# Kernel optimization log

Measured on AMD Instinct MI355X. Metric: run time of the kernel, lower is better.

Reference implementation:

```python
import jax, jax.numpy as jnp
import numpy as np

N_HEAD = 16
HEAD_DIM = 128  # n_embd // n_head
RMS_EPS = 1.1920929e-07  # torch.finfo(float32).eps, F.rms_norm default
ROPE_BASE = 10000.0


def _rope_tables(T, head_dim, dtype=jnp.float32):
    half = head_dim // 2
    inv_freq = 1.0 / (ROPE_BASE ** (jnp.arange(half, dtype=jnp.float32) / half))
    t = jnp.arange(T, dtype=jnp.float32)
    freqs = jnp.outer(t, inv_freq)  # [T, half]
    return jnp.cos(freqs).astype(dtype), jnp.sin(freqs).astype(dtype)


def _apply_rope(x, cos, sin):
    # x: [B, T, H, D]; cos/sin: [T, D//2]
    half = x.shape[-1] // 2
    x1, x2 = x[..., :half], x[..., half:]
    c = cos[None, :, None, :]
    s = sin[None, :, None, :]
    return jnp.concatenate([x1 * c - x2 * s, x1 * s + x2 * c], axis=-1)


def _rms_norm(x):
    ms = jnp.mean(jnp.square(x), axis=-1, keepdims=True)
    return x * jax.lax.rsqrt(ms + RMS_EPS)


def setup_inputs() -> dict:
    key = jax.random.key(0)
    ks = jax.random.split(key, 5)
    B, T, E = 4, 2048, 2048
    x = jax.random.normal(ks[0], (B, T, E), dtype=jnp.float32)
    scale = 0.02
    wq = jax.random.normal(ks[1], (E, E), dtype=jnp.float32) * scale
    wk = jax.random.normal(ks[2], (E, E), dtype=jnp.float32) * scale
    wv = jax.random.normal(ks[3], (E, E), dtype=jnp.float32) * scale
    wo = jax.random.normal(ks[4], (E, E), dtype=jnp.float32) * scale
    return {"x": x, "wq": wq, "wk": wk, "wv": wv, "wo": wo}


def reference(x, wq, wk, wv, wo):
    B, T, E = x.shape
    H, D = N_HEAD, HEAD_DIM
    # QKV projections (bias-free linears)
    q = (x @ wq).reshape(B, T, H, D)
    k = (x @ wk).reshape(B, T, H, D)
    v = (x @ wv).reshape(B, T, H, D)
    # RoPE then parameter-free QK RMS norm
    cos, sin = _rope_tables(T, D, x.dtype)
    q = _rms_norm(_apply_rope(q, cos, sin))
    k = _rms_norm(_apply_rope(k, cos, sin))
    # causal SDPA
    scale = 1.0 / jnp.sqrt(jnp.asarray(D, dtype=x.dtype))
    scores = jnp.einsum('bqhd,bkhd->bhqk', q, k) * scale
    causal = jnp.tril(jnp.ones((T, T), dtype=bool))
    scores = jnp.where(causal[None, None], scores, jnp.asarray(-jnp.inf, scores.dtype))
    attn = jax.nn.softmax(scores, axis=-1)
    y = jnp.einsum('bhqk,bkhd->bqhd', attn, v).reshape(B, T, E)
    return y @ wo
```

## Files before the change

kernel.cpp:

```cpp
#include <hip/hip_runtime.h>
#include <math.h>

#define T_SEQ 2048
#define BATCH 4
#define E_DIM 2048
#define NHEAD 16
#define HDIM 128
#define RMS_EPS 1.1920929e-07f
#define NQT (T_SEQ / 128)

typedef unsigned short u16;
typedef __attribute__((ext_vector_type(8))) unsigned short u16x8;
typedef __attribute__((ext_vector_type(8))) short bf16x8;
typedef __attribute__((ext_vector_type(4))) float f32x4;

typedef const __attribute__((address_space(1))) unsigned int g_u32;
typedef __attribute__((address_space(3))) unsigned int l_u32;

static __device__ __forceinline__ u16 f2b(float f) {
  unsigned int u = __builtin_bit_cast(unsigned int, f);
  u += 0x7fffu + ((u >> 16) & 1u);
  return (u16)(u >> 16);
}
static __device__ __forceinline__ float b2f(u16 v) {
  return __builtin_bit_cast(float, ((unsigned int)v) << 16);
}

__global__ __launch_bounds__(256) void convert_f32_bf16(
    const float* __restrict__ src, u16* __restrict__ dst, int n) {
  int i = (blockIdx.x * 256 + threadIdx.x) * 4;
  if (i >= n) return;
  float4 v = *reinterpret_cast<const float4*>(src + i);
  ushort4 o;
  o.x = f2b(v.x); o.y = f2b(v.y); o.z = f2b(v.z); o.w = f2b(v.w);
  *reinterpret_cast<ushort4*>(dst + i) = o;
}

__global__ __launch_bounds__(256) void convt_w_k(
    const float* __restrict__ W, u16* __restrict__ Wt) {
  __shared__ u16 tile[64][72];
  int c0 = blockIdx.x * 64;
  int r0 = blockIdx.y * 64;
  int tid = threadIdx.x;
  int lrow = tid >> 2;
  int lcol = (tid & 3) * 16;
#pragma unroll
  for (int i = 0; i < 4; ++i) {
    float4 v = *reinterpret_cast<const float4*>(
        W + (long long)(r0 + lrow) * E_DIM + c0 + lcol + i * 4);
    tile[lrow][lcol + i * 4 + 0] = f2b(v.x);
    tile[lrow][lcol + i * 4 + 1] = f2b(v.y);
    tile[lrow][lcol + i * 4 + 2] = f2b(v.z);
    tile[lrow][lcol + i * 4 + 3] = f2b(v.w);
  }
  __syncthreads();
  int wrow = tid >> 2;
  int wcol = (tid & 3) * 16;
  u16 o[16];
#pragma unroll
  for (int i = 0; i < 16; ++i) o[i] = tile[wcol + i][wrow];
  u16* dst = Wt + (long long)(c0 + wrow) * E_DIM + r0 + wcol;
  *reinterpret_cast<u16x8*>(dst)     = *reinterpret_cast<u16x8*>(&o[0]);
  *reinterpret_cast<u16x8*>(dst + 8) = *reinterpret_cast<u16x8*>(&o[8]);
}

__global__ __launch_bounds__(256) void rope_tables_k(
    float* __restrict__ cost, float* __restrict__ sint) {
  int idx = blockIdx.x * 256 + threadIdx.x;
  int i = idx & 63, t = idx >> 6;
  double inv = pow(10000.0, -(double)i / 64.0);
  double ang = (double)t * inv;
  cost[idx] = (float)cos(ang);
  sint[idx] = (float)sin(ang);
}

__global__ __launch_bounds__(256) void rope_rms_k(
    u16* __restrict__ Qb, u16* __restrict__ Kb, const float* __restrict__ cost,
    const float* __restrict__ sint) {
  int half = gridDim.x >> 1;
  int isK = blockIdx.x >= half;
  u16* qk = isK ? Kb : Qb;
  float outscale = isK ? 1.0f : 0.08838834764831845f;
  int wave = threadIdx.x >> 6;
  int lane = threadIdx.x & 63;
  long long row = (long long)(blockIdx.x - (isK ? half : 0)) * 4 + wave;
  int th = (int)(row >> 4);
  int t = th & (T_SEQ - 1);
  u16* p = qk + row * HDIM;
  float x1 = b2f(p[lane]);
  float x2 = b2f(p[lane + 64]);
  float c = cost[t * 64 + lane];
  float s = sint[t * 64 + lane];
  float o1 = x1 * c - x2 * s;
  float o2 = x1 * s + x2 * c;
  float ss = o1 * o1 + o2 * o2;
#pragma unroll
  for (int m = 32; m >= 1; m >>= 1) ss += __shfl_xor(ss, m, 64);
  float r = rsqrtf(ss * (1.0f / 128.0f) + RMS_EPS) * outscale;
  p[lane] = f2b(o1 * r);
  p[lane + 64] = f2b(o2 * r);
}

__global__ __launch_bounds__(256) void transpose_v_k(
    const u16* __restrict__ V, u16* __restrict__ Vt) {
  __shared__ u16 tile[64][72];
  int t0 = blockIdx.x * 64, d0 = blockIdx.y * 64;
  int bh = blockIdx.z;
  int b = bh >> 4, h = bh & 15;
  int tid = threadIdx.x;
  int lrow = tid >> 3;
  int lcol = (tid & 7) * 8;
#pragma unroll
  for (int pass = 0; pass < 2; ++pass) {
    int row = lrow + pass * 32;
    const u16* src = V + ((((long long)b * T_SEQ + t0 + row) * NHEAD + h) << 7) + d0 + lcol;
    *reinterpret_cast<u16x8*>(&tile[row][lcol]) = *reinterpret_cast<const u16x8*>(src);
  }
  __syncthreads();
#pragma unroll
  for (int pass = 0; pass < 2; ++pass) {
    int drow = (tid >> 3) + pass * 32;
    int tcol = (tid & 7) * 8;
    u16x8 o;
#pragma unroll
    for (int i = 0; i < 8; ++i) o[i] = tile[tcol + i][drow];
    u16* dst = Vt + ((long long)bh * HDIM + d0 + drow) * T_SEQ + t0 + tcol;
    *reinterpret_cast<u16x8*>(dst) = o;
  }
}

__global__ __launch_bounds__(512, 2) void gemm_bt_k(
    const u16* __restrict__ A,
    const u16* __restrict__ Bt0, const u16* __restrict__ Bt1, const u16* __restrict__ Bt2,
    u16* __restrict__ C0, u16* __restrict__ C1, u16* __restrict__ C2,
    float* __restrict__ Cf, int M, int N, int K) {
  int lin = blockIdx.x + (blockIdx.y << 3) + (blockIdx.z << 8);
  int kx = lin & 7, ii = lin >> 3;
  int by = ((kx >> 1) << 3) + (ii & 7);
  int bx, bz;
  if (gridDim.z == 3) {
    int u = (kx & 1) * 12 + (ii >> 3);
    bx = u & 7; bz = u >> 3;
  } else {
    bx = ((kx & 1) << 2) + (ii >> 3);
    bz = 0;
  }
  const u16* Bt = bz == 0 ? Bt0 : (bz == 1 ? Bt1 : Bt2);
  u16* C = bz == 0 ? C0 : (bz == 1 ? C1 : C2);

  __shared__ u16 As[2][256 * 64];
  __shared__ u16 Bs[2][256 * 64];
  const int tid = threadIdx.x;
  const int lane = tid & 63, wave = tid >> 6;
  const int wm = wave >> 2, wn = wave & 3;
  const int m0 = by * 256, n0 = bx * 256;
  const int lr = lane & 15, lq = lane >> 4, l7 = lane & 7;
  const int NT = K >> 6;

  int rowA[2][2], rowB[2][2];
  const u16* gA[2][2];
  const u16* gB[2][2];
#pragma unroll
  for (int l = 0; l < 2; ++l) {
    int rihb = l * 64 + wave * 8;
#pragma unroll
    for (int h = 0; h < 2; ++h) {
      int ra = ((rihb >> 6) << 7) + h * 64 + (rihb & 63);
      int rb = ((rihb >> 5) << 6) + h * 32 + (rihb & 31);
      rowA[h][l] = ra;
      rowB[h][l] = rb;
      int rA = ra + (lane >> 3);
      int rB = rb + (lane >> 3);
      gA[h][l] = A + (long long)(m0 + rA) * K + ((l7 ^ (rA & 7)) * 8);
      gB[h][l] = Bt + (long long)(n0 + rB) * K + ((l7 ^ (rB & 7)) * 8);
    }
  }

  f32x4 acc[8][4] = {};

#define GLDS(gp, lp) \
  __builtin_amdgcn_global_load_lds((g_u32*)(gp), (l_u32*)(lp), 16, 0, 0)
#define LD_A(mt, ks)                                                          \
  (*reinterpret_cast<const bf16x8*>(                                          \
      Ab + (wm * 128 + (mt) * 16 + lr) * 64 + ((((ks) << 2) + lq) ^ l7) * 8))
#define LD_B(nt, ks)                                                          \
  (*reinterpret_cast<const bf16x8*>(                                          \
      Bb + (wn * 64 + (nt) * 16 + lr) * 64 + ((((ks) << 2) + lq) ^ l7) * 8))
#define MFMA_PH(ph)                                                           \
  _Pragma("unroll") for (int mi = 0; mi < 2; ++mi)                            \
  _Pragma("unroll") for (int ni = 0; ni < 4; ++ni)                            \
  _Pragma("unroll") for (int ks = 0; ks < 2; ++ks)                            \
    acc[(ph) * 2 + mi][ni] = __builtin_amdgcn_mfma_f32_16x16x32_bf16(         \
        aA[mi][ks], bB[ni][ks], acc[(ph) * 2 + mi][ni], 0, 0, 0);

  GLDS(gB[0][0], &Bs[0][rowB[0][0] * 64]); GLDS(gB[0][1], &Bs[0][rowB[0][1] * 64]);
  GLDS(gB[1][0], &Bs[0][rowB[1][0] * 64]); GLDS(gB[1][1], &Bs[0][rowB[1][1] * 64]);
  GLDS(gA[0][0], &As[0][rowA[0][0] * 64]); GLDS(gA[0][1], &As[0][rowA[0][1] * 64]);
  GLDS(gA[1][0], &As[0][rowA[1][0] * 64]); GLDS(gA[1][1], &As[0][rowA[1][1] * 64]);
  GLDS(gB[0][0] + 64, &Bs[1][rowB[0][0] * 64]); GLDS(gB[0][1] + 64, &Bs[1][rowB[0][1] * 64]);
  GLDS(gB[1][0] + 64, &Bs[1][rowB[1][0] * 64]); GLDS(gB[1][1] + 64, &Bs[1][rowB[1][1] * 64]);
  GLDS(gA[0][0] + 64, &As[1][rowA[0][0] * 64]); GLDS(gA[0][1] + 64, &As[1][rowA[0][1] * 64]);
  asm volatile("s_waitcnt vmcnt(6)" ::: "memory");
  __builtin_amdgcn_s_barrier();
  __builtin_amdgcn_sched_barrier(0);

  for (int t = 0; t < NT; ++t) {
    const u16* Ab = As[t & 1];
    const u16* Bb = Bs[t & 1];
    u16* An = (u16*)As[(t & 1) ^ 1];
    u16* Ac = (u16*)As[t & 1];
    u16* Bc = (u16*)Bs[t & 1];
    const bool g1 = (t + 1 < NT), g2 = (t + 2 < NT);
    bf16x8 aA[2][2], bB[4][2];

#pragma unroll
    for (int mi = 0; mi < 2; ++mi) { aA[mi][0] = LD_A(mi, 0); aA[mi][1] = LD_A(mi, 1); }
#pragma unroll
    for (int ni = 0; ni < 4; ++ni) { bB[ni][0] = LD_B(ni, 0); bB[ni][1] = LD_B(ni, 1); }
    if (g1) {
      GLDS(gA[1][0] + 64, &An[rowA[1][0] * 64]);
      GLDS(gA[1][1] + 64, &An[rowA[1][1] * 64]);
    }
    asm volatile("s_waitcnt lgkmcnt(8)" ::: "memory");
    __builtin_amdgcn_s_barrier();
    asm volatile("s_waitcnt lgkmcnt(0)" ::: "memory");
    __builtin_amdgcn_sched_barrier(0);
    __builtin_amdgcn_s_setprio(1);
    MFMA_PH(0);
    __builtin_amdgcn_s_setprio(0);
    __builtin_amdgcn_s_barrier();

#pragma unroll
    for (int mi = 0; mi < 2; ++mi) { aA[mi][0] = LD_A(2 + mi, 0); aA[mi][1] = LD_A(2 + mi, 1); }
    if (g2) {
      GLDS(gB[0][0] + 128, &Bc[rowB[0][0] * 64]);
      GLDS(gB[0][1] + 128, &Bc[rowB[0][1] * 64]);
    }
    __builtin_amdgcn_s_barrier();
    asm volatile("s_waitcnt lgkmcnt(0)" ::: "memory");
    __builtin_amdgcn_sched_barrier(0);
    __builtin_amdgcn_s_setprio(1);
    MFMA_PH(1);
    __builtin_amdgcn_s_setprio(0);
    __builtin_amdgcn_s_barrier();

#pragma unroll
    for (int mi = 0; mi < 2; ++mi) { aA[mi][0] = LD_A(4 + mi, 0); aA[mi][1] = LD_A(4 + mi, 1); }
    if (g2) {
      GLDS(gB[1][0] + 128, &Bc[rowB[1][0] * 64]);
      GLDS(gB[1][1] + 128, &Bc[rowB[1][1] * 64]);
    }
    __builtin_amdgcn_s_barrier();
    asm volatile("s_waitcnt lgkmcnt(0)" ::: "memory");
    __builtin_amdgcn_sched_barrier(0);
    __builtin_amdgcn_s_setprio(1);
    MFMA_PH(2);
    __builtin_amdgcn_s_setprio(0);
    __builtin_amdgcn_s_barrier();

#pragma unroll
    for (int mi = 0; mi < 2; ++mi) { aA[mi][0] = LD_A(6 + mi, 0); aA[mi][1] = LD_A(6 + mi, 1); }
    if (g2) {
      GLDS(gA[0][0] + 128, &Ac[rowA[0][0] * 64]);
      GLDS(gA[0][1] + 128, &Ac[rowA[0][1] * 64]);
    }
    __builtin_amdgcn_s_barrier();
    asm volatile("s_waitcnt lgkmcnt(0)" ::: "memory");
    __builtin_amdgcn_sched_barrier(0);
    __builtin_amdgcn_s_setprio(1);
    MFMA_PH(3);
    __builtin_amdgcn_s_setprio(0);
    if (t < NT - 2) {
      asm volatile("s_waitcnt vmcnt(6)" ::: "memory");
    } else {
      asm volatile("s_waitcnt vmcnt(0)" ::: "memory");
    }
    __builtin_amdgcn_s_barrier();
    __builtin_amdgcn_sched_barrier(0);

#pragma unroll
    for (int l = 0; l < 2; ++l)
#pragma unroll
      for (int h = 0; h < 2; ++h) { gA[h][l] += 64; gB[h][l] += 64; }
  }
#undef LD_A
#undef LD_B
#undef MFMA_PH
#undef GLDS

#pragma unroll
  for (int mt = 0; mt < 8; ++mt)
#pragma unroll
    for (int nt = 0; nt < 4; ++nt) {
      long long col = n0 + wn * 64 + nt * 16 + lr;
#pragma unroll
      for (int r = 0; r < 4; ++r) {
        long long row = m0 + wm * 128 + mt * 16 + lq * 4 + r;
        float v = acc[mt][nt][r];
        if (Cf) Cf[row * N + col] = v;
        else C[row * N + col] = f2b(v);
      }
    }
}

__global__ __launch_bounds__(256, 3) void attn_k(
    const u16* __restrict__ Q, const u16* __restrict__ K,
    const u16* __restrict__ Vt, u16* __restrict__ Y) {
  __shared__ u16 Ks[64 * 128];
  __shared__ u16 Vs[128 * 64];
  __shared__ u16 Ps[4][32 * 72];
  __shared__ float Al[4][32];
  int lin = blockIdx.x + (blockIdx.y << 3);
  int pair = (lin >> 6);
  int bh = ((lin & 7) << 3) + ((lin >> 3) & 7);
  int b = bh >> 4, h = bh & 15;
  int tid = threadIdx.x, lane = tid & 63, wave = tid >> 6;
  int lr = lane & 15, lq = lane >> 4;

  const u16* kp[4];
  const u16* vp[4];
#pragma unroll
  for (int p = 0; p < 4; ++p) {
    int c = p * 256 + wave * 64 + lane;
    int key = c >> 4, sk = c & 15, gk = (sk - key) & 15;
    kp[p] = K + (((long long)b * T_SEQ + key) * NHEAD + h) * HDIM + gk * 8;
    int d = c >> 3, sv = c & 7, gv = (sv - d) & 7;
    vp[p] = Vt + ((long long)bh * HDIM + d) * T_SEQ + gv * 8;
  }

#pragma unroll 1
  for (int phase = 0; phase < 2; ++phase) {
    int qt = phase == 0 ? (NQT - 1 - pair) : pair;
    int qbase = qt * 128 + wave * 32;

    bf16x8 aq[2][4];
#pragma unroll
    for (int n2 = 0; n2 < 2; ++n2) {
      const u16* qp = Q + (((long long)b * T_SEQ + qbase + n2 * 16 + lr) * NHEAD + h) * HDIM;
#pragma unroll
      for (int kt = 0; kt < 4; ++kt)
        aq[n2][kt] = *reinterpret_cast<const bf16x8*>(qp + kt * 32 + lq * 8);
    }

    float m_s[2], l_s[2];
#pragma unroll
    for (int n2 = 0; n2 < 2; ++n2) { m_s[n2] = -INFINITY; l_s[n2] = 0.f; }
    f32x4 o[2][8] = {};

    int niter = 2 * qt + 2;
    for (int j = 0; j < niter; ++j) {
      __syncthreads();
#pragma unroll
      for (int p = 0; p < 4; ++p) {
        __builtin_amdgcn_global_load_lds(
            (g_u32*)(kp[p] + (long long)j * 64 * NHEAD * HDIM),
            (l_u32*)(Ks + p * 2048 + wave * 512), 16, 0, 0);
        __builtin_amdgcn_global_load_lds(
            (g_u32*)(vp[p] + j * 64),
            (l_u32*)(Vs + p * 2048 + wave * 512), 16, 0, 0);
      }
      __syncthreads();

      f32x4 s[4][2];
#pragma unroll
      for (int mt = 0; mt < 4; ++mt) {
        int key = mt * 16 + lr;
        bf16x8 ak[4];
#pragma unroll
        for (int kt = 0; kt < 4; ++kt) {
          int slot = (kt * 4 + lq + key) & 15;
          ak[kt] = *reinterpret_cast<const bf16x8*>(&Ks[key * 128 + slot * 8]);
        }
#pragma unroll
        for (int n2 = 0; n2 < 2; ++n2) {
          f32x4 acc = {};
#pragma unroll
          for (int kt = 0; kt < 4; ++kt)
            acc = __builtin_amdgcn_mfma_f32_16x16x32_bf16(ak[kt], aq[n2][kt], acc, 0, 0, 0);
          s[mt][n2] = acc;
        }
      }

      if (j >= 2 * qt) {
#pragma unroll
        for (int mt = 0; mt < 4; ++mt)
#pragma unroll
          for (int n2 = 0; n2 < 2; ++n2) {
            int q = qbase + n2 * 16 + lr;
#pragma unroll
            for (int r = 0; r < 4; ++r) {
              int key = j * 64 + mt * 16 + lq * 4 + r;
              if (key > q) s[mt][n2][r] = -INFINITY;
            }
          }
      }

      float alpha[2];
#pragma unroll
      for (int n2 = 0; n2 < 2; ++n2) {
        float mx = s[0][n2][0];
#pragma unroll
        for (int mt = 0; mt < 4; ++mt)
#pragma unroll
          for (int r = 0; r < 4; ++r) mx = fmaxf(mx, s[mt][n2][r]);
        mx = fmaxf(mx, __shfl_xor(mx, 16, 64));
        mx = fmaxf(mx, __shfl_xor(mx, 32, 64));
        float mn = fmaxf(m_s[n2], mx);
        alpha[n2] = __expf(m_s[n2] - mn);
        m_s[n2] = mn;
        float sum = 0.f;
        int q = n2 * 16 + lr;
#pragma unroll
        for (int mt = 0; mt < 4; ++mt) {
          ushort4 pk;
          float p0 = __expf(s[mt][n2][0] - mn);
          float p1 = __expf(s[mt][n2][1] - mn);
          float p2 = __expf(s[mt][n2][2] - mn);
          float p3 = __expf(s[mt][n2][3] - mn);
          sum += (p0 + p1) + (p2 + p3);
          pk.x = f2b(p0); pk.y = f2b(p1); pk.z = f2b(p2); pk.w = f2b(p3);
          *reinterpret_cast<ushort4*>(&Ps[wave][q * 72 + mt * 16 + lq * 4]) = pk;
        }
        sum += __shfl_xor(sum, 16, 64);
        sum += __shfl_xor(sum, 32, 64);
        l_s[n2] = l_s[n2] * alpha[n2] + sum;
      }

      if (lq == 0) {
        Al[wave][lr] = alpha[0];
        Al[wave][16 + lr] = alpha[1];
      }
#pragma unroll
      for (int q2 = 0; q2 < 2; ++q2) {
        f32x4 av = *reinterpret_cast<const f32x4*>(&Al[wave][q2 * 16 + lq * 4]);
#pragma unroll
        for (int r = 0; r < 4; ++r)
#pragma unroll
          for (int dt = 0; dt < 8; ++dt) o[q2][dt][r] *= av[r];
      }

#pragma unroll
      for (int kh = 0; kh < 2; ++kh) {
        bf16x8 ap[2];
#pragma unroll
        for (int q2 = 0; q2 < 2; ++q2)
          ap[q2] = *reinterpret_cast<const bf16x8*>(
              &Ps[wave][(q2 * 16 + lr) * 72 + kh * 32 + lq * 8]);
#pragma unroll
        for (int dt = 0; dt < 8; ++dt) {
          int d = dt * 16 + lr;
          int slot = (kh * 4 + lq + d) & 7;
          bf16x8 bv = *reinterpret_cast<const bf16x8*>(&Vs[d * 64 + slot * 8]);
#pragma unroll
          for (int q2 = 0; q2 < 2; ++q2)
            o[q2][dt] = __builtin_amdgcn_mfma_f32_16x16x32_bf16(ap[q2], bv, o[q2][dt], 0, 0, 0);
        }
      }
    }

    if (lq == 0) {
      Al[wave][lr] = l_s[0];
      Al[wave][16 + lr] = l_s[1];
    }
#pragma unroll
    for (int q2 = 0; q2 < 2; ++q2) {
      f32x4 lv = *reinterpret_cast<const f32x4*>(&Al[wave][q2 * 16 + lq * 4]);
#pragma unroll
      for (int r = 0; r < 4; ++r) {
        float inv = 1.0f / lv[r];
        int q = qbase + q2 * 16 + lq * 4 + r;
        u16* yp = Y + (((long long)b * T_SEQ + q) * NHEAD + h) * HDIM;
#pragma unroll
        for (int dt = 0; dt < 8; ++dt)
          yp[dt * 16 + lr] = f2b(o[q2][dt][r] * inv);
      }
    }
  }
}

extern "C" void kernel_launch(void* const* d_in, const int* in_sizes, int n_in,
                              void* d_out, int out_size, void* d_ws, size_t ws_size,
                              hipStream_t stream) {
  (void)in_sizes; (void)n_in; (void)out_size; (void)ws_size;
  const float* x  = (const float*)d_in[0];
  const float* wq = (const float*)d_in[1];
  const float* wk = (const float*)d_in[2];
  const float* wv = (const float*)d_in[3];
  const float* wo = (const float*)d_in[4];
  float* out = (float*)d_out;

  char* ws = (char*)d_ws;
  size_t off = 0;
  auto alloc = [&](size_t bytes) {
    char* p = ws + off;
    off += (bytes + 255) & ~(size_t)255;
    return p;
  };
  const size_t NTOK = (size_t)BATCH * T_SEQ;
  const size_t XE = NTOK * E_DIM;
  const size_t WE = (size_t)E_DIM * E_DIM;

  u16* xb  = (u16*)alloc(XE * 2);
  u16* wqt = (u16*)alloc(WE * 2);
  u16* wkt = (u16*)alloc(WE * 2);
  u16* wvt = (u16*)alloc(WE * 2);
  u16* wot = (u16*)alloc(WE * 2);
  u16* Qb  = (u16*)alloc(XE * 2);
  u16* Kb  = (u16*)alloc(XE * 2);
  u16* Vb  = (u16*)alloc(XE * 2);
  u16* Vt  = (u16*)alloc(XE * 2);
  u16* Yb  = (u16*)alloc(XE * 2);
  float* cost = (float*)alloc((size_t)T_SEQ * 64 * 4);
  float* sint = (float*)alloc((size_t)T_SEQ * 64 * 4);

  convert_f32_bf16<<<XE / 1024, 256, 0, stream>>>(x, xb, (int)XE);
  dim3 gw(E_DIM / 64, E_DIM / 64);
  convt_w_k<<<gw, 256, 0, stream>>>(wq, wqt);
  convt_w_k<<<gw, 256, 0, stream>>>(wk, wkt);
  convt_w_k<<<gw, 256, 0, stream>>>(wv, wvt);
  convt_w_k<<<gw, 256, 0, stream>>>(wo, wot);
  rope_tables_k<<<(T_SEQ * 64) / 256, 256, 0, stream>>>(cost, sint);

  dim3 gq(E_DIM / 256, NTOK / 256, 3);
  gemm_bt_k<<<gq, 512, 0, stream>>>(xb, wqt, wkt, wvt, Qb, Kb, Vb, nullptr,
                                    (int)NTOK, E_DIM, E_DIM);

  rope_rms_k<<<(unsigned)(NTOK * NHEAD / 4) * 2, 256, 0, stream>>>(Qb, Kb, cost, sint);

  dim3 gt(T_SEQ / 64, HDIM / 64, BATCH * NHEAD);
  transpose_v_k<<<gt, 256, 0, stream>>>(Vb, Vt);

  dim3 ga(NQT / 2, BATCH * NHEAD);
  attn_k<<<ga, 256, 0, stream>>>(Qb, Kb, Vt, Yb);

  dim3 go(E_DIM / 256, NTOK / 256, 1);
  gemm_bt_k<<<go, 512, 0, stream>>>(Yb, wot, wot, wot, nullptr, nullptr, nullptr, out,
                                    (int)NTOK, E_DIM, E_DIM);
}
```

Measured before the change: 655.7 us.

## Software-pipeline LDS fragment loads one phase ahead in GEMM main loop

Restructures the bf16 GEMM main loop to unroll two K-tiles per iteration, with double-buffered register fragments (aX/aY, bU/bV). Each phase's LDS reads are issued before the previous phase's MFMAs, so LDS latency is hidden behind matrix math instead of waiting on lgkmcnt(0). Global-to-LDS staging and vmcnt waits are rescheduled to match. The cost is higher register pressure, which may hurt occupancy under launch bounds, plus a more fragile barrier and waitcnt ordering.

```diff
diff --git a/kernel.cpp b/kernel.cpp
--- a/kernel.cpp
+++ b/kernel.cpp
@@ -150,6 +150,8 @@
 
   __shared__ u16 As[2][256 * 64];
   __shared__ u16 Bs[2][256 * 64];
+  u16* A0 = As[0]; u16* A1 = As[1];
+  u16* B0 = Bs[0]; u16* B1 = Bs[1];
   const int tid = threadIdx.x;
   const int lane = tid & 63, wave = tid >> 6;
   const int wm = wave >> 2, wn = wave & 3;
@@ -177,116 +179,95 @@
   }
 
   f32x4 acc[8][4] = {};
+  bf16x8 aX[2][2], aY[2][2], bU[4][2], bV[4][2];
 
 #define GLDS(gp, lp) \
   __builtin_amdgcn_global_load_lds((g_u32*)(gp), (l_u32*)(lp), 16, 0, 0)
-#define LD_A(mt, ks)                                                          \
-  (*reinterpret_cast<const bf16x8*>(                                          \
-      Ab + (wm * 128 + (mt) * 16 + lr) * 64 + ((((ks) << 2) + lq) ^ l7) * 8))
-#define LD_B(nt, ks)                                                          \
-  (*reinterpret_cast<const bf16x8*>(                                          \
-      Bb + (wn * 64 + (nt) * 16 + lr) * 64 + ((((ks) << 2) + lq) ^ l7) * 8))
-#define MFMA_PH(ph)                                                           \
+#define STG_A(bufp, h, off) do {                                              \
+    GLDS(gA[h][0] + (off), (bufp) + rowA[h][0] * 64);                         \
+    GLDS(gA[h][1] + (off), (bufp) + rowA[h][1] * 64); } while (0)
+#define STG_B(bufp, h, off) do {                                              \
+    GLDS(gB[h][0] + (off), (bufp) + rowB[h][0] * 64);                         \
+    GLDS(gB[h][1] + (off), (bufp) + rowB[h][1] * 64); } while (0)
+#define LDSA(dst, buf, mtb)                                                   \
+  _Pragma("unroll") for (int mi = 0; mi < 2; ++mi)                            \
+  _Pragma("unroll") for (int ks = 0; ks < 2; ++ks)                            \
+    dst[mi][ks] = *reinterpret_cast<const bf16x8*>(                           \
+        (buf) + (wm * 128 + ((mtb) + mi) * 16 + lr) * 64 +                    \
+        ((((ks) << 2) + lq) ^ l7) * 8);
+#define LDSB(dst, buf)                                                        \
+  _Pragma("unroll") for (int ni = 0; ni < 4; ++ni)                            \
+  _Pragma("unroll") for (int ks = 0; ks < 2; ++ks)                            \
+    dst[ni][ks] = *reinterpret_cast<const bf16x8*>(                           \
+        (buf) + (wn * 64 + (ni) * 16 + lr) * 64 +                             \
+        ((((ks) << 2) + lq) ^ l7) * 8);
+#define MFMA2(ph, a, b)                                                       \
   _Pragma("unroll") for (int mi = 0; mi < 2; ++mi)                            \
   _Pragma("unroll") for (int ni = 0; ni < 4; ++ni)                            \
   _Pragma("unroll") for (int ks = 0; ks < 2; ++ks)                            \
     acc[(ph) * 2 + mi][ni] = __builtin_amdgcn_mfma_f32_16x16x32_bf16(         \
-        aA[mi][ks], bB[ni][ks], acc[(ph) * 2 + mi][ni], 0, 0, 0);
-
-  GLDS(gB[0][0], &Bs[0][rowB[0][0] * 64]); GLDS(gB[0][1], &Bs[0][rowB[0][1] * 64]);
-  GLDS(gB[1][0], &Bs[0][rowB[1][0] * 64]); GLDS(gB[1][1], &Bs[0][rowB[1][1] * 64]);
-  GLDS(gA[0][0], &As[0][rowA[0][0] * 64]); GLDS(gA[0][1], &As[0][rowA[0][1] * 64]);
-  GLDS(gA[1][0], &As[0][rowA[1][0] * 64]); GLDS(gA[1][1], &As[0][rowA[1][1] * 64]);
-  GLDS(gB[0][0] + 64, &Bs[1][rowB[0][0] * 64]); GLDS(gB[0][1] + 64, &Bs[1][rowB[0][1] * 64]);
-  GLDS(gB[1][0] + 64, &Bs[1][rowB[1][0] * 64]); GLDS(gB[1][1] + 64, &Bs[1][rowB[1][1] * 64]);
-  GLDS(gA[0][0] + 64, &As[1][rowA[0][0] * 64]); GLDS(gA[0][1] + 64, &As[1][rowA[0][1] * 64]);
-  asm volatile("s_waitcnt vmcnt(6)" ::: "memory");
-  __builtin_amdgcn_s_barrier();
-  __builtin_amdgcn_sched_barrier(0);
-
-  for (int t = 0; t < NT; ++t) {
-    const u16* Ab = As[t & 1];
-    const u16* Bb = Bs[t & 1];
-    u16* An = (u16*)As[(t & 1) ^ 1];
-    u16* Ac = (u16*)As[t & 1];
-    u16* Bc = (u16*)Bs[t & 1];
-    const bool g1 = (t + 1 < NT), g2 = (t + 2 < NT);
-    bf16x8 aA[2][2], bB[4][2];
-
-#pragma unroll
-    for (int mi = 0; mi < 2; ++mi) { aA[mi][0] = LD_A(mi, 0); aA[mi][1] = LD_A(mi, 1); }
-#pragma unroll
-    for (int ni = 0; ni < 4; ++ni) { bB[ni][0] = LD_B(ni, 0); bB[ni][1] = LD_B(ni, 1); }
-    if (g1) {
-      GLDS(gA[1][0] + 64, &An[rowA[1][0] * 64]);
-      GLDS(gA[1][1] + 64, &An[rowA[1][1] * 64]);
-    }
-    asm volatile("s_waitcnt lgkmcnt(8)" ::: "memory");
-    __builtin_amdgcn_s_barrier();
-    asm volatile("s_waitcnt lgkmcnt(0)" ::: "memory");
-    __builtin_amdgcn_sched_barrier(0);
-    __builtin_amdgcn_s_setprio(1);
-    MFMA_PH(0);
-    __builtin_amdgcn_s_setprio(0);
-    __builtin_amdgcn_s_barrier();
-
-#pragma unroll
-    for (int mi = 0; mi < 2; ++mi) { aA[mi][0] = LD_A(2 + mi, 0); aA[mi][1] = LD_A(2 + mi, 1); }
-    if (g2) {
-      GLDS(gB[0][0] + 128, &Bc[rowB[0][0] * 64]);
-      GLDS(gB[0][1] + 128, &Bc[rowB[0][1] * 64]);
-    }
-    __builtin_amdgcn_s_barrier();
-    asm volatile("s_waitcnt lgkmcnt(0)" ::: "memory");
-    __builtin_amdgcn_sched_barrier(0);
-    __builtin_amdgcn_s_setprio(1);
-    MFMA_PH(1);
-    __builtin_amdgcn_s_setprio(0);
-    __builtin_amdgcn_s_barrier();
-
-#pragma unroll
-    for (int mi = 0; mi < 2; ++mi) { aA[mi][0] = LD_A(4 + mi, 0); aA[mi][1] = LD_A(4 + mi, 1); }
-    if (g2) {
-      GLDS(gB[1][0] + 128, &Bc[rowB[1][0] * 64]);
-      GLDS(gB[1][1] + 128, &Bc[rowB[1][1] * 64]);
-    }
-    __builtin_amdgcn_s_barrier();
-    asm volatile("s_waitcnt lgkmcnt(0)" ::: "memory");
-    __builtin_amdgcn_sched_barrier(0);
-    __builtin_amdgcn_s_setprio(1);
-    MFMA_PH(2);
-    __builtin_amdgcn_s_setprio(0);
-    __builtin_amdgcn_s_barrier();
-
-#pragma unroll
-    for (int mi = 0; mi < 2; ++mi) { aA[mi][0] = LD_A(6 + mi, 0); aA[mi][1] = LD_A(6 + mi, 1); }
-    if (g2) {
-      GLDS(gA[0][0] + 128, &Ac[rowA[0][0] * 64]);
-      GLDS(gA[0][1] + 128, &Ac[rowA[0][1] * 64]);
-    }
-    __builtin_amdgcn_s_barrier();
-    asm volatile("s_waitcnt lgkmcnt(0)" ::: "memory");
-    __builtin_amdgcn_sched_barrier(0);
-    __builtin_amdgcn_s_setprio(1);
-    MFMA_PH(3);
-    __builtin_amdgcn_s_setprio(0);
-    if (t < NT - 2) {
-      asm volatile("s_waitcnt vmcnt(6)" ::: "memory");
-    } else {
-      asm volatile("s_waitcnt vmcnt(0)" ::: "memory");
-    }
-    __builtin_amdgcn_s_barrier();
-    __builtin_amdgcn_sched_barrier(0);
-
+        a[mi][ks], b[ni][ks], acc[(ph) * 2 + mi][ni], 0, 0, 0);
+#define SB __builtin_amdgcn_sched_barrier(0)
+#define BAR __builtin_amdgcn_s_barrier()
+#define VMC(n) asm volatile("s_waitcnt vmcnt(" #n ")" ::: "memory")
+#define PH_MID SB; BAR; SB; __builtin_amdgcn_s_setprio(1)
+#define PH_END __builtin_amdgcn_s_setprio(0); SB; BAR; SB
+
+  GLDS(gB[0][0], B0 + rowB[0][0] * 64); GLDS(gB[0][1], B0 + rowB[0][1] * 64);
+  GLDS(gB[1][0], B0 + rowB[1][0] * 64); GLDS(gB[1][1], B0 + rowB[1][1] * 64);
+  GLDS(gA[0][0], A0 + rowA[0][0] * 64); GLDS(gA[0][1], A0 + rowA[0][1] * 64);
+  GLDS(gA[1][0], A0 + rowA[1][0] * 64); GLDS(gA[1][1], A0 + rowA[1][1] * 64);
+  GLDS(gB[0][0] + 64, B1 + rowB[0][0] * 64); GLDS(gB[0][1] + 64, B1 + rowB[0][1] * 64);
+  GLDS(gB[1][0] + 64, B1 + rowB[1][0] * 64); GLDS(gB[1][1] + 64, B1 + rowB[1][1] * 64);
+  GLDS(gA[0][0] + 64, A1 + rowA[0][0] * 64); GLDS(gA[0][1] + 64, A1 + rowA[0][1] * 64);
+  VMC(6);
+  BAR; SB;
+  LDSB(bU, B0);
+  LDSA(aX, A0, 0);
+  SB;
+
+#pragma unroll 1
+  for (int t = 0; t < NT; t += 2) {
+    const bool nl = (t + 2 < NT);
+    LDSA(aY, A0, 2);
+    STG_A(A1, 1, 64);
+    PH_MID; MFMA2(0, aX, bU); PH_END;
+    LDSA(aX, A0, 4);
+    if (nl) { STG_B(B0, 0, 128); VMC(6); } else { VMC(4); }
+    PH_MID; MFMA2(1, aY, bU); PH_END;
+    LDSA(aY, A0, 6);
+    LDSB(bV, B1);
+    if (nl) { STG_B(B0, 1, 128); VMC(4); } else { VMC(0); }
+    PH_MID; MFMA2(2, aX, bU); PH_END;
+    LDSA(aX, A1, 0);
+    if (nl) STG_A(A0, 0, 128);
+    PH_MID; MFMA2(3, aY, bU); PH_END;
+    LDSA(aY, A1, 2);
+    if (nl) STG_A(A0, 1, 128);
+    PH_MID; MFMA2(0, aX, bV); PH_END;
+    LDSA(aX, A1, 4);
+    if (nl) { STG_B(B1, 0, 192); VMC(6); }
+    PH_MID; MFMA2(1, aY, bV); PH_END;
+    LDSA(aY, A1, 6);
+    LDSB(bU, B0);
+    if (nl) { STG_B(B1, 1, 192); VMC(4); }
+    PH_MID; MFMA2(2, aX, bV); PH_END;
+    LDSA(aX, A0, 0);
+    if (nl) STG_A(A1, 0, 192);
+    PH_MID; MFMA2(3, aY, bV); PH_END;
 #pragma unroll
     for (int l = 0; l < 2; ++l)
 #pragma unroll
-      for (int h = 0; h < 2; ++h) { gA[h][l] += 64; gB[h][l] += 64; }
-  }
-#undef LD_A
-#undef LD_B
-#undef MFMA_PH
+      for (int h = 0; h < 2; ++h) { gA[h][l] += 128; gB[h][l] += 128; }
+  }
+#undef LDSA
+#undef LDSB
+#undef MFMA2
+#undef STG_A
+#undef STG_B
 #undef GLDS
+#undef PH_MID
+#undef PH_END
 
 #pragma unroll
   for (int mt = 0; mt < 8; ++mt)
```

New measurement: 786.6 us. 1.2x slower.
